# Optimization experiments

Hardware: AMD Instinct MI355X
Metric: run time of the kernel (lower is better)

The kernel has to match this reference:

```python
import jax, jax.numpy as jnp
import numpy as np

DIM = 1024
NUM_EXPERTS = 4
NUM_HEADS = 16
MLP_RATIO = 4
B, N = 8, 1024
EPS = 1e-5


def layernorm(x, w, b):
    mu = jnp.mean(x, axis=-1, keepdims=True)
    var = jnp.mean(jnp.square(x - mu), axis=-1, keepdims=True)
    return (x - mu) * jax.lax.rsqrt(var + EPS) * w + b


def setup_inputs() -> dict:
    key = jax.random.key(0)
    ks = jax.random.split(key, 6)
    x = jax.random.normal(ks[0], (B, N, DIM), dtype=jnp.float32)
    expert_mask = jax.random.randint(ks[1], (B, N), 0, NUM_EXPERTS)
    expert_probs = jax.random.uniform(ks[2], (B, N), dtype=jnp.float32)
    expand_dim = 3 * DIM + MLP_RATIO * DIM
    expand_weight = jax.random.normal(ks[3], (expand_dim, DIM), dtype=jnp.float32) * 0.02
    mlp_bias = jnp.zeros((MLP_RATIO * DIM,), dtype=jnp.float32)
    contract_weight = jax.random.normal(ks[4], (2 * DIM, MLP_RATIO * DIM + DIM), dtype=jnp.float32) * 0.02
    contract_bias = jnp.zeros((2 * DIM,), dtype=jnp.float32)
    norm1_w = jnp.ones((DIM,), dtype=jnp.float32)
    norm1_b = jnp.zeros((DIM,), dtype=jnp.float32)
    norm2_w = jnp.ones((2 * DIM,), dtype=jnp.float32)
    norm2_b = jnp.zeros((2 * DIM,), dtype=jnp.float32)
    return {"x": x, "expert_probs": expert_probs, "expand_weight": expand_weight,
            "mlp_bias": mlp_bias, "contract_weight": contract_weight,
            "contract_bias": contract_bias, "norm1_w": norm1_w, "norm1_b": norm1_b,
            "norm2_w": norm2_w, "norm2_b": norm2_b, "expert_mask": expert_mask}


def reference(x, expert_probs, expand_weight, mlp_bias, contract_weight,
              contract_bias, norm1_w, norm1_b, norm2_w, norm2_b, expert_mask):
    dim = DIM
    # nested sub-dim per token: expert m uses first dim >> (E-1-m) features
    shift = NUM_EXPERTS - 1 - expert_mask                       # (B, N)
    d_in = dim // jnp.left_shift(1, shift)                      # (B, N)
    in_mask = (jnp.arange(dim)[None, None, :] < d_in[..., None]).astype(x.dtype)

    # fused expand bias: [mlp_bias, qkv_bias(=zeros since qkv_bias=False)]
    input_bias = jnp.concatenate([mlp_bias, jnp.zeros((3 * dim,), x.dtype)], axis=-1)

    xn = layernorm(x, norm1_w, norm1_b) * in_mask               # nested_linear_expand input masking
    y = jnp.einsum('bnd,ed->bne', xn, expand_weight) + input_bias  # (B, N, 7*dim)

    qkv, mlp_hidden = y[..., :3 * dim], y[..., 3 * dim:]
    q = qkv[..., :dim]
    kv = layernorm(qkv[..., dim:], norm2_w, norm2_b)            # (B, N, 2*dim)
    k, v = kv[..., :dim], kv[..., dim:]

    # multi-head attention
    dh = dim // NUM_HEADS
    scale = dh ** -0.5
    b, n = x.shape[0], x.shape[1]
    def heads(t):
        return t.reshape(b, n, NUM_HEADS, dh).transpose(0, 2, 1, 3)
    qh, kh, vh = heads(q), heads(k), heads(v)
    attn = jax.nn.softmax(jnp.einsum('bhqd,bhkd->bhqk', qh, kh) * scale, axis=-1)
    attn_output = jnp.einsum('bhqk,bhkd->bhqd', attn, vh).transpose(0, 2, 1, 3).reshape(b, n, dim)

    # nested_linear_contract: full matmul, then mask outputs beyond (2*dim)>>shift
    concat_in = jnp.concatenate([jax.nn.gelu(mlp_hidden, approximate=False), attn_output], axis=-1)
    cy = jnp.einsum('bnc,oc->bno', concat_in, contract_weight) + contract_bias  # (B, N, 2*dim)
    d_out = (2 * dim) // jnp.left_shift(1, shift)
    out_mask = (jnp.arange(2 * dim)[None, None, :] < d_out[..., None]).astype(x.dtype)
    cy = cy * out_mask + jnp.concatenate([x, x], axis=-1)       # residual.repeat(1,1,2)

    mlp_output, attn_out = cy[..., :dim], cy[..., dim:]
    return attn_out + expert_probs[..., None] * mlp_output
```

## Files before the change

kernel.cpp:

```cpp
#include <hip/hip_runtime.h>
#include <cmath>

#define NT    8192
#define DIM_  1024
#define EXP_  7168
#define CD_   5120
#define OD_   2048
#define MPAD  8704
#define NRT   68

typedef __attribute__((ext_vector_type(8))) short short8;
typedef __attribute__((ext_vector_type(4))) float f32x4;
typedef __attribute__((ext_vector_type(4))) unsigned short ushort4_t;

__device__ __forceinline__ unsigned short f2bf(float f) {
  union { float f; unsigned u; } v; v.f = f;
  return (unsigned short)((v.u + 0x7FFFu + ((v.u >> 16) & 1u)) >> 16);
}
__device__ __forceinline__ float bf2f(unsigned short u) {
  union { unsigned u; float f; } v; v.u = ((unsigned)u) << 16;
  return v.f;
}

#define MFMA16(a, b, c) __builtin_amdgcn_mfma_f32_16x16x32_bf16(a, b, c, 0, 0, 0)

__global__ __launch_bounds__(256) void count_experts(const int* __restrict__ em,
                                                     int* __restrict__ blockCnt) {
  __shared__ int h[4];
  int tid = threadIdx.x;
  if (tid < 4) h[tid] = 0;
  __syncthreads();
  atomicAdd(&h[em[blockIdx.x * 256 + tid]], 1);
  __syncthreads();
  if (tid < 4) blockCnt[blockIdx.x * 4 + tid] = h[tid];
}

__global__ void scan_make(const int* __restrict__ blockCnt, int* __restrict__ desc) {
  if (threadIdx.x != 0) return;
  int cnt[4] = {0, 0, 0, 0};
  for (int b = 0; b < 32; b++)
    for (int e = 0; e < 4; e++) cnt[e] += blockCnt[b * 4 + e];
  int base[4]; int acc = 0;
  for (int e = 0; e < 4; e++) { base[e] = acc; acc += ((cnt[e] + 127) >> 7) << 7; }
  for (int e = 0; e < 4; e++) { desc[e] = base[e]; desc[4 + e] = cnt[e]; }
  for (int r = 0; r < NRT; r++) {
    int te = -1;
    for (int e = 0; e < 4; e++) {
      int lo = base[e] >> 7;
      int hi = (base[e] + (((cnt[e] + 127) >> 7) << 7)) >> 7;
      if (r >= lo && r < hi) te = e;
    }
    desc[8 + r] = te;
  }
  int run[4];
  for (int e = 0; e < 4; e++) run[e] = base[e];
  for (int b = 0; b < 32; b++)
    for (int e = 0; e < 4; e++) { desc[76 + b * 4 + e] = run[e]; run[e] += blockCnt[b * 4 + e]; }
}

__global__ __launch_bounds__(256) void fill_perm(int* __restrict__ perm) {
  int i = blockIdx.x * 256 + threadIdx.x;
  if (i < MPAD) perm[i] = -1;
}

__global__ __launch_bounds__(256) void scatter_perm(const int* __restrict__ em,
    const int* __restrict__ desc, int* __restrict__ perm, int* __restrict__ pos) {
  __shared__ int wsum[4][4];
  int tid = threadIdx.x;
  int wv = tid >> 6, ln = tid & 63;
  int t = blockIdx.x * 256 + tid;
  int e = em[t];
  int wrank = 0;
#pragma unroll
  for (int k = 0; k < 4; k++) {
    unsigned long long m = __ballot(e == k);
    if (ln == 0) wsum[wv][k] = __popcll(m);
    if (e == k) wrank = __popcll(m & ((1ull << ln) - 1ull));
  }
  __syncthreads();
  int off = desc[76 + blockIdx.x * 4 + e];
  for (int w = 0; w < wv; w++) off += wsum[w][e];
  int p = off + wrank;
  perm[p] = t;
  pos[t] = p;
}

__global__ __launch_bounds__(256) void cvt_bf16(const float* __restrict__ in,
                                                unsigned short* __restrict__ out, int n) {
  int i = (blockIdx.x * 256 + threadIdx.x) * 4;
  if (i >= n) return;
  float4 v = *(const float4*)(in + i);
  ushort4_t o;
  o[0] = f2bf(v.x); o[1] = f2bf(v.y); o[2] = f2bf(v.z); o[3] = f2bf(v.w);
  *(ushort4_t*)(out + i) = o;
}

__global__ __launch_bounds__(256) void ln1_kernel(const float* __restrict__ x,
    const float* __restrict__ w, const float* __restrict__ b,
    const int* __restrict__ emask, const int* __restrict__ pos,
    unsigned short* __restrict__ xn) {
  int wave = threadIdx.x >> 6, lane = threadIdx.x & 63;
  int t = blockIdx.x * 4 + wave;
  const float* xt = x + (size_t)t * DIM_;
  float4 v[4];
  float s = 0.f, s2 = 0.f;
#pragma unroll
  for (int i = 0; i < 4; i++) {
    v[i] = *(const float4*)(xt + i * 256 + lane * 4);
    s  += v[i].x + v[i].y + v[i].z + v[i].w;
    s2 += v[i].x * v[i].x + v[i].y * v[i].y + v[i].z * v[i].z + v[i].w * v[i].w;
  }
#pragma unroll
  for (int o = 1; o < 64; o <<= 1) { s += __shfl_xor(s, o); s2 += __shfl_xor(s2, o); }
  float mu = s * (1.f / 1024.f);
  float rs = rsqrtf(s2 * (1.f / 1024.f) - mu * mu + 1e-5f);
  int din = 1024 >> (3 - emask[t]);
  unsigned short* ot = xn + (size_t)pos[t] * DIM_;
#pragma unroll
  for (int i = 0; i < 4; i++) {
    int c0 = i * 256 + lane * 4;
    float fv[4] = { v[i].x, v[i].y, v[i].z, v[i].w };
    ushort4_t o;
#pragma unroll
    for (int j = 0; j < 4; j++) {
      int c = c0 + j;
      float val = (c < din) ? (fv[j] - mu) * rs * w[c] + b[c] : 0.f;
      o[j] = f2bf(val);
    }
    *(ushort4_t*)(ot + c0) = o;
  }
}

__global__ __launch_bounds__(256, 3) void gemm_grp1(
    const unsigned short* __restrict__ A, const unsigned short* __restrict__ W,
    const float* __restrict__ bias, const int* __restrict__ tdesc,
    const int* __restrict__ perm, unsigned short* __restrict__ out0,
    unsigned short* __restrict__ out1, unsigned short* __restrict__ out2) {
  __shared__ unsigned short lds[16384];
  unsigned short* As = lds;
  unsigned short* Bs = lds + 8192;
  const int r = blockIdx.y;
  const int e = tdesc[8 + r];
  if (e < 0) return;
  const int ntiles = 4 << e;
  constexpr int KK = 1024;

  const int tid = threadIdx.x;
  const int lane = tid & 63;
  const int wave = tid >> 6;
  const int wm = wave >> 1, wn = wave & 1;
  const int lg = lane >> 4, lr = lane & 15;

  constexpr int CPX = 56 >> 3;
  const int bx = (int)blockIdx.x;
  const int bn = (bx & 7) * CPX + (bx >> 3);
  const int n0 = bn * 128;
  const int m0 = r * 128;

  const int s0g = tid >> 3,        s1g = (256 + tid) >> 3;
  const int lc0 = (tid & 7) ^ (s0g & 7), lc1 = (tid & 7) ^ (s1g & 7);
  const int row0 = 2 * s0g + (lc0 >> 2), kc0 = lc0 & 3;
  const int row1 = 2 * s1g + (lc1 >> 2), kc1 = lc1 & 3;
  const unsigned short* aS0 = A + (size_t)(m0 + row0) * KK + kc0 * 8;
  const unsigned short* aS1 = A + (size_t)(m0 + row1) * KK + kc1 * 8;
  const unsigned short* bS0 = W + (size_t)(n0 + row0) * KK + kc0 * 8;
  const unsigned short* bS1 = W + (size_t)(n0 + row1) * KK + kc1 * 8;

#define GLD(SRC, DST)                                                                \
  __builtin_amdgcn_global_load_lds(                                                  \
      (const __attribute__((address_space(1))) void*)(SRC),                          \
      (__attribute__((address_space(3))) void*)(DST), 16, 0, 0)
#define STAGE(T, SLOT) {                                                             \
    GLD(aS0 + (size_t)(T) * 32, As + (SLOT) * 4096 + tid * 8);                       \
    GLD(aS1 + (size_t)(T) * 32, As + (SLOT) * 4096 + 2048 + tid * 8);                \
    GLD(bS0 + (size_t)(T) * 32, Bs + (SLOT) * 4096 + tid * 8);                       \
    GLD(bS1 + (size_t)(T) * 32, Bs + (SLOT) * 4096 + 2048 + tid * 8);                \
  }

  const int fb = (lr >> 1) * 128 + ((((lr & 1) << 2) + lg) ^ ((lr >> 1) & 7)) * 16;
  const char* apb = (const char*)As + wm * 4096 + fb;
  const char* bpb = (const char*)Bs + wn * 4096 + fb;

  short8 afr[4], bfr[4];
#define LDFRAG(C)                                                                    \
  _Pragma("unroll") for (int mi = 0; mi < 4; mi++)                                   \
    afr[mi] = *(const short8*)(apb + (C) * 8192 + mi * 1024);                        \
  _Pragma("unroll") for (int ni = 0; ni < 4; ni++)                                   \
    bfr[ni] = *(const short8*)(bpb + (C) * 8192 + ni * 1024);

  f32x4 acc[4][4];
  f32x4 zf = { 0.f, 0.f, 0.f, 0.f };
#pragma unroll
  for (int i = 0; i < 4; i++)
#pragma unroll
    for (int j = 0; j < 4; j++) acc[i][j] = zf;

  STAGE(0, 0)
  STAGE(1, 1)
  asm volatile("s_waitcnt vmcnt(4)" ::: "memory");
  __builtin_amdgcn_s_barrier();

#pragma unroll 1
  for (int t = 0; t < ntiles; ++t) {
    const int c = t & 1;
    LDFRAG(c)
    asm volatile("s_waitcnt lgkmcnt(0)" ::: "memory");
    __builtin_amdgcn_sched_barrier(0);
    __builtin_amdgcn_s_barrier();
    const int t2 = (t + 2 < ntiles) ? t + 2 : t;
    STAGE(t2, c)
    __builtin_amdgcn_s_setprio(1);
#pragma unroll
    for (int mi = 0; mi < 4; mi++)
#pragma unroll
      for (int ni = 0; ni < 4; ni++)
        acc[mi][ni] = MFMA16(afr[mi], bfr[ni], acc[mi][ni]);
    __builtin_amdgcn_s_setprio(0);
    asm volatile("s_waitcnt vmcnt(4)" ::: "memory");
    __builtin_amdgcn_s_barrier();
  }
  asm volatile("s_waitcnt vmcnt(0)" ::: "memory");

#pragma unroll
  for (int mi = 0; mi < 4; mi++) {
#pragma unroll
    for (int ni = 0; ni < 4; ni++) {
#pragma unroll
      for (int rr = 0; rr < 4; rr++) {
        int grow = m0 + wm * 64 + mi * 16 + lg * 4 + rr;
        int gcol = n0 + wn * 64 + ni * 16 + lr;
        float v = acc[mi][ni][rr];
        int tk = perm[grow];
        if (tk < 0) continue;
        float bv = bias[gcol & 4095];
        v += (gcol < 4096) ? bv : 0.f;
        if (gcol < 1024) {
          int bb = tk >> 10, n = tk & 1023, h = gcol >> 6, d = gcol & 63;
          out0[(((size_t)(bb * 16 + h) * 1024 + n) << 6) + d] = f2bf(v * 0.125f);
        } else if (gcol < 3072) {
          out1[(size_t)tk * OD_ + (gcol - 1024)] = f2bf(v);
        } else {
          float g = 0.5f * v * (1.f + erff(v * 0.70710678f));
          out2[(size_t)tk * CD_ + (gcol - 3072)] = f2bf(g);
        }
      }
    }
  }
#undef GLD
#undef STAGE
#undef LDFRAG
}

__global__ __launch_bounds__(512, 2) void gemm2_8p(
    const unsigned short* __restrict__ A, const unsigned short* __restrict__ W,
    const float* __restrict__ bias, unsigned short* __restrict__ out0) {
  extern __shared__ unsigned short lds[];
  unsigned short* As = lds;
  unsigned short* Bs = lds + 32768;
  constexpr int KK = 5120;
  constexpr int NTILES = KK / 64;
  const int tid = threadIdx.x;
  const int lane = tid & 63;
  const int wave = tid >> 6;
  const int wm = wave >> 2;
  const int wn = wave & 3;
  const int lg = lane >> 4, lr = lane & 15;

  int cpx = (int)gridDim.x >> 3;
  int lid = ((int)blockIdx.x & 7) * cpx + ((int)blockIdx.x >> 3);
  int bm = lid >> 3, bn = lid & 7;
  int m0 = bm * 256, n0 = bn * 256;

  const int srow = tid >> 3;
  const int schunk = (tid & 7) ^ (srow & 7);
  const unsigned short* aSrc = A + (size_t)(m0 + srow) * KK + schunk * 8;
  const unsigned short* bSrc = W + (size_t)(n0 + srow) * KK + schunk * 8;

  const int xor0 = (lg ^ (lr & 7)) * 8;
  const int xor1 = ((4 + lg) ^ (lr & 7)) * 8;
  const unsigned short* ap0 = As + (wm * 64 + lr) * 64 + xor0;
  const unsigned short* ap1 = As + (wm * 64 + lr) * 64 + xor1;
  const unsigned short* bp0 = Bs + (wn * 32 + lr) * 64 + xor0;
  const unsigned short* bp1 = Bs + (wn * 32 + lr) * 64 + xor1;

#define STAGE_A(TT, SLOT, SEG)                                                       \
  __builtin_amdgcn_global_load_lds(                                                  \
    (const __attribute__((address_space(1))) void*)(aSrc +                           \
      (size_t)(SEG) * 64 * KK + (size_t)(TT) * 64),                                  \
    (__attribute__((address_space(3))) void*)(As + (SLOT) * 16384 +                  \
      (SEG) * 4096 + tid * 8), 16, 0, 0)
#define STAGE_B(TT, SLOT, SEG)                                                       \
  __builtin_amdgcn_global_load_lds(                                                  \
    (const __attribute__((address_space(1))) void*)(bSrc +                           \
      (size_t)(SEG) * 64 * KK + (size_t)(TT) * 64),                                  \
    (__attribute__((address_space(3))) void*)(Bs + (SLOT) * 16384 +                  \
      (SEG) * 4096 + tid * 8), 16, 0, 0)

  short8 afr[4][2], bfr[2][2][2];
#define LDFRAG_A(C, QM)                                                              \
  _Pragma("unroll") for (int mi = 0; mi < 4; mi++) {                                 \
    afr[mi][0] = *(const short8*)(ap0 + (C) * 16384 + (QM) * 8192 + mi * 1024);      \
    afr[mi][1] = *(const short8*)(ap1 + (C) * 16384 + (QM) * 8192 + mi * 1024);      \
  }
#define LDFRAG_B(C, QN)                                                              \
  _Pragma("unroll") for (int ni = 0; ni < 2; ni++) {                                 \
    bfr[QN][ni][0] = *(const short8*)(bp0 + (C) * 16384 + (QN) * 8192 + ni * 1024);  \
    bfr[QN][ni][1] = *(const short8*)(bp1 + (C) * 16384 + (QN) * 8192 + ni * 1024);  \
  }
#define DOMFMA(QM, QN)                                                               \
  __builtin_amdgcn_s_setprio(1);                                                     \
  _Pragma("unroll") for (int mi = 0; mi < 4; mi++)                                   \
  _Pragma("unroll") for (int ni = 0; ni < 2; ni++) {                                 \
    acc[(QM) * 4 + mi][(QN) * 2 + ni] =                                              \
        MFMA16(afr[mi][0], bfr[QN][ni][0], acc[(QM) * 4 + mi][(QN) * 2 + ni]);       \
    acc[(QM) * 4 + mi][(QN) * 2 + ni] =                                              \
        MFMA16(afr[mi][1], bfr[QN][ni][1], acc[(QM) * 4 + mi][(QN) * 2 + ni]);       \
  }                                                                                  \
  __builtin_amdgcn_s_setprio(0);

#define SCHED0 __builtin_amdgcn_sched_barrier(0)

#define TILE_BODY(T, C) {                                                            \
    const int tn1 = ((T) + 1 < NTILES) ? (T) + 1 : NTILES - 1;                       \
    const int tn2 = ((T) + 2 < NTILES) ? (T) + 2 : NTILES - 1;                       \
    LDFRAG_A(C, 0); LDFRAG_B(C, 0);                                                  \
    STAGE_B(tn1, (C) ^ 1, 2); STAGE_B(tn1, (C) ^ 1, 3);                              \
    SCHED0;                                                                          \
    __builtin_amdgcn_s_barrier();                                                    \
    asm volatile("s_waitcnt lgkmcnt(0)");                                            \
    SCHED0;                                                                          \
    DOMFMA(0, 0);                                                                    \
    asm volatile("s_waitcnt vmcnt(6)" ::: "memory");                                 \
    __builtin_amdgcn_s_barrier();                                                    \
    LDFRAG_B(C, 1);                                                                  \
    STAGE_A(tn1, (C) ^ 1, 2); STAGE_A(tn1, (C) ^ 1, 3);                              \
    SCHED0;                                                                          \
    __builtin_amdgcn_s_barrier();                                                    \
    asm volatile("s_waitcnt lgkmcnt(0)");                                            \
    SCHED0;                                                                          \
    DOMFMA(0, 1);                                                                    \
    __builtin_amdgcn_s_barrier();                                                    \
    LDFRAG_A(C, 1);                                                                  \
    STAGE_A(tn2, (C), 0); STAGE_A(tn2, (C), 1);                                      \
    SCHED0;                                                                          \
    __builtin_amdgcn_s_barrier();                                                    \
    asm volatile("s_waitcnt lgkmcnt(0)");                                            \
    SCHED0;                                                                          \
    DOMFMA(1, 0);                                                                    \
    __builtin_amdgcn_s_barrier();                                                    \
    STAGE_B(tn2, (C), 0); STAGE_B(tn2, (C), 1);                                      \
    SCHED0;                                                                          \
    __builtin_amdgcn_s_barrier();                                                    \
    DOMFMA(1, 1);                                                                    \
    asm volatile("s_waitcnt vmcnt(8)" ::: "memory");                                 \
    __builtin_amdgcn_s_barrier();                                                    \
  }

  f32x4 acc[8][4];
  f32x4 zf = { 0.f, 0.f, 0.f, 0.f };
#pragma unroll
  for (int i = 0; i < 8; i++)
#pragma unroll
    for (int j = 0; j < 4; j++) acc[i][j] = zf;

  STAGE_A(0, 0, 0); STAGE_A(0, 0, 1); STAGE_A(0, 0, 2); STAGE_A(0, 0, 3);
  STAGE_B(0, 0, 0); STAGE_B(0, 0, 1); STAGE_B(0, 0, 2); STAGE_B(0, 0, 3);
  STAGE_A(1, 1, 0); STAGE_A(1, 1, 1);
  STAGE_B(1, 1, 0); STAGE_B(1, 1, 1);
  asm volatile("s_waitcnt vmcnt(4)" ::: "memory");
  __builtin_amdgcn_s_barrier();

#pragma unroll 1
  for (int tp = 0; tp < NTILES / 2; ++tp) {
    TILE_BODY(2 * tp, 0)
    TILE_BODY(2 * tp + 1, 1)
  }
  asm volatile("s_waitcnt vmcnt(0)" ::: "memory");

#pragma unroll
  for (int mi8 = 0; mi8 < 8; mi8++) {
#pragma unroll
    for (int nj = 0; nj < 4; nj++) {
#pragma unroll
      for (int r = 0; r < 4; r++) {
        int grow = m0 + wm * 64 + (mi8 >> 2) * 128 + (mi8 & 3) * 16 + lg * 4 + r;
        int gcol = n0 + wn * 32 + (nj >> 1) * 128 + (nj & 1) * 16 + lr;
        float v = acc[mi8][nj][r] + bias[gcol];
        out0[(size_t)grow * OD_ + gcol] = f2bf(v);
      }
    }
  }
#undef STAGE_A
#undef STAGE_B
#undef LDFRAG_A
#undef LDFRAG_B
#undef DOMFMA
#undef SCHED0
#undef TILE_BODY
}

__global__ __launch_bounds__(256) void ln2_kernel(const unsigned short* __restrict__ kv,
    const float* __restrict__ w, const float* __restrict__ b,
    unsigned short* __restrict__ kb, unsigned short* __restrict__ vrm) {
  int wave = threadIdx.x >> 6, lane = threadIdx.x & 63;
  int t = blockIdx.x * 4 + wave;
  const unsigned short* p = kv + (size_t)t * OD_;
  float vals[4][8];
  float s = 0.f, s2 = 0.f;
#pragma unroll
  for (int i = 0; i < 4; i++) {
    short8 v = *(const short8*)(p + i * 512 + lane * 8);
#pragma unroll
    for (int j = 0; j < 8; j++) {
      float f = bf2f((unsigned short)v[j]);
      vals[i][j] = f; s += f; s2 += f * f;
    }
  }
#pragma unroll
  for (int o = 1; o < 64; o <<= 1) { s += __shfl_xor(s, o); s2 += __shfl_xor(s2, o); }
  float mu = s * (1.f / 2048.f);
  float rs = rsqrtf(s2 * (1.f / 2048.f) - mu * mu + 1e-5f);
  int bidx = t >> 10, n = t & 1023;
#pragma unroll
  for (int i = 0; i < 4; i++) {
    int c0 = i * 512 + lane * 8;
    short8 o8;
#pragma unroll
    for (int j = 0; j < 8; j++) {
      int c = c0 + j;
      o8[j] = (short)f2bf((vals[i][j] - mu) * rs * w[c] + b[c]);
    }
    if (c0 < 1024) {
      int h = c0 >> 6, d = c0 & 63;
      *(short8*)(kb + (((size_t)(bidx * 16 + h) * 1024 + n) << 6) + d) = o8;
    } else {
      *(short8*)(vrm + (size_t)t * 1024 + (c0 - 1024)) = o8;
    }
  }
}

__global__ __launch_bounds__(256) void transpose_v(const unsigned short* __restrict__ vrm,
                                                   unsigned short* __restrict__ vt) {
  int bh = blockIdx.x >> 4;
  int nblk = (blockIdx.x & 15) * 64;
  int b = bh >> 4, h = bh & 15;
  __shared__ unsigned short tile[64][65];
  int tid = threadIdx.x;
  int i = tid >> 2;
  int d0 = (tid & 3) * 16;
  const unsigned short* src = vrm + ((size_t)(b * 1024 + nblk + i)) * 1024 + h * 64 + d0;
  short8 v0 = *(const short8*)(src);
  short8 v1 = *(const short8*)(src + 8);
#pragma unroll
  for (int j = 0; j < 8; j++) {
    tile[d0 + j][i] = (unsigned short)v0[j];
    tile[d0 + 8 + j][i] = (unsigned short)v1[j];
  }
  __syncthreads();
  int d = tid >> 2;
  int i0 = (tid & 3) * 16;
  unsigned short* dst = vt + ((size_t)bh * 64 + d) * 1024 + nblk + i0;
  short8 o0, o1;
#pragma unroll
  for (int j = 0; j < 8; j++) { o0[j] = (short)tile[d][i0 + j]; o1[j] = (short)tile[d][i0 + 8 + j]; }
  *(short8*)dst = o0;
  *(short8*)(dst + 8) = o1;
}

__global__ __launch_bounds__(64) void attn_kernel(const unsigned short* __restrict__ q,
    const unsigned short* __restrict__ k, const unsigned short* __restrict__ vt,
    unsigned short* __restrict__ concat) {
  int bh = blockIdx.x >> 5;
  int q0 = (blockIdx.x & 31) * 32;
  int lane = threadIdx.x;
  int lg = lane >> 4, lr = lane & 15;
  __shared__ unsigned short plds[2][512];
  const unsigned short* qp = q + (size_t)bh * (1024 * 64);
  const unsigned short* kp = k + (size_t)bh * (1024 * 64);
  const unsigned short* vp = vt + (size_t)bh * (64 * 1024);
  short8 qf[2][2];
#pragma unroll
  for (int rb = 0; rb < 2; rb++)
#pragma unroll
    for (int c = 0; c < 2; c++)
      qf[rb][c] = *(const short8*)(qp + (q0 + rb * 16 + lr) * 64 + c * 32 + lg * 8);
  f32x4 zf = { 0.f, 0.f, 0.f, 0.f };
  f32x4 o[2][4];
  float m[2][4], l[2][4];
#pragma unroll
  for (int rb = 0; rb < 2; rb++) {
#pragma unroll
    for (int r = 0; r < 4; r++) { m[rb][r] = -1e30f; l[rb][r] = 0.f; }
#pragma unroll
    for (int nb = 0; nb < 4; nb++) o[rb][nb] = zf;
  }
  for (int kt = 0; kt < 1024; kt += 32) {
    f32x4 s[2][2];
    s[0][0] = zf; s[0][1] = zf; s[1][0] = zf; s[1][1] = zf;
#pragma unroll
    for (int h2 = 0; h2 < 2; h2++) {
      short8 kf0 = *(const short8*)(kp + (kt + h2 * 16 + lr) * 64 + lg * 8);
      short8 kf1 = *(const short8*)(kp + (kt + h2 * 16 + lr) * 64 + 32 + lg * 8);
      s[0][h2] = MFMA16(qf[0][0], kf0, s[0][h2]);
      s[0][h2] = MFMA16(qf[0][1], kf1, s[0][h2]);
      s[1][h2] = MFMA16(qf[1][0], kf0, s[1][h2]);
      s[1][h2] = MFMA16(qf[1][1], kf1, s[1][h2]);
    }
    __syncthreads();
#pragma unroll
    for (int rb = 0; rb < 2; rb++) {
      float mx[4], rsum[4];
#pragma unroll
      for (int r = 0; r < 4; r++) mx[r] = fmaxf(s[rb][0][r], s[rb][1][r]);
#pragma unroll
      for (int ofs = 1; ofs < 16; ofs <<= 1)
#pragma unroll
        for (int r = 0; r < 4; r++) mx[r] = fmaxf(mx[r], __shfl_xor(mx[r], ofs));
#pragma unroll
      for (int r = 0; r < 4; r++) {
        float mn = fmaxf(m[rb][r], mx[r]);
        float al = __expf(m[rb][r] - mn);
        float p0 = __expf(s[rb][0][r] - mn);
        float p1 = __expf(s[rb][1][r] - mn);
        m[rb][r] = mn;
        plds[rb][(lg * 4 + r) * 32 + lr] = f2bf(p0);
        plds[rb][(lg * 4 + r) * 32 + 16 + lr] = f2bf(p1);
        rsum[r] = p0 + p1;
        l[rb][r] *= al;
#pragma unroll
        for (int nb = 0; nb < 4; nb++) o[rb][nb][r] *= al;
      }
#pragma unroll
      for (int ofs = 1; ofs < 16; ofs <<= 1)
#pragma unroll
        for (int r = 0; r < 4; r++) rsum[r] += __shfl_xor(rsum[r], ofs);
#pragma unroll
      for (int r = 0; r < 4; r++) l[rb][r] += rsum[r];
    }
    __syncthreads();
    short8 pf0 = *(const short8*)(&plds[0][lr * 32 + lg * 8]);
    short8 pf1 = *(const short8*)(&plds[1][lr * 32 + lg * 8]);
#pragma unroll
    for (int nb = 0; nb < 4; nb++) {
      short8 vf = *(const short8*)(vp + (nb * 16 + lr) * 1024 + kt + lg * 8);
      o[0][nb] = MFMA16(pf0, vf, o[0][nb]);
      o[1][nb] = MFMA16(pf1, vf, o[1][nb]);
    }
  }
  int b = bh >> 4, h = bh & 15;
#pragma unroll
  for (int rb = 0; rb < 2; rb++)
#pragma unroll
    for (int r = 0; r < 4; r++) {
      int n = q0 + rb * 16 + lg * 4 + r;
      size_t t = (size_t)b * 1024 + n;
      float inv = 1.f / l[rb][r];
#pragma unroll
      for (int nb = 0; nb < 4; nb++)
        concat[t * CD_ + 4096 + h * 64 + nb * 16 + lr] = f2bf(o[rb][nb][r] * inv);
    }
}

__global__ __launch_bounds__(256) void final_epi(const unsigned short* __restrict__ cy,
    const float* __restrict__ x, const float* __restrict__ probs,
    const int* __restrict__ emask, float* __restrict__ out) {
  int t = blockIdx.x;
  int c = threadIdx.x * 4;
  int dout = 2048 >> (3 - emask[t]);
  float p = probs[t];
  const unsigned short* cyt = cy + (size_t)t * OD_;
  ushort4_t mv = *(const ushort4_t*)(cyt + c);
  ushort4_t av = *(const ushort4_t*)(cyt + 1024 + c);
  float4 xv = *(const float4*)(x + (size_t)t * 1024 + c);
  float xa[4] = { xv.x, xv.y, xv.z, xv.w };
  float4 o;
  float oa[4];
#pragma unroll
  for (int j = 0; j < 4; j++) {
    float mlp = ((c + j) < dout ? bf2f(mv[j]) : 0.f) + xa[j];
    float att = ((1024 + c + j) < dout ? bf2f(av[j]) : 0.f) + xa[j];
    oa[j] = att + p * mlp;
  }
  o.x = oa[0]; o.y = oa[1]; o.z = oa[2]; o.w = oa[3];
  *(float4*)(out + (size_t)t * 1024 + c) = o;
}

extern "C" void kernel_launch(void* const* d_in, const int* in_sizes, int n_in,
                              void* d_out, int out_size, void* d_ws, size_t ws_size,
                              hipStream_t stream) {
  const float* x        = (const float*)d_in[0];
  const float* probs    = (const float*)d_in[1];
  const float* we       = (const float*)d_in[2];
  const float* mlp_bias = (const float*)d_in[3];
  const float* wc       = (const float*)d_in[4];
  const float* cbias    = (const float*)d_in[5];
  const float* n1w      = (const float*)d_in[6];
  const float* n1b      = (const float*)d_in[7];
  const float* n2w      = (const float*)d_in[8];
  const float* n2b      = (const float*)d_in[9];
  const int*   emask    = (const int*)d_in[10];
  float* out = (float*)d_out;

  char* ws = (char*)d_ws;
  size_t off = 0;
  auto alloc = [&](size_t bytes) {
    char* p = ws + off;
    off += (bytes + 255) & ~(size_t)255;
    return p;
  };
  unsigned short* we_bf = (unsigned short*)alloc((size_t)EXP_ * DIM_ * 2);
  unsigned short* wc_bf = (unsigned short*)alloc((size_t)OD_ * CD_ * 2);
  unsigned short* xn    = (unsigned short*)alloc((size_t)MPAD * DIM_ * 2);
  unsigned short* qb    = (unsigned short*)alloc((size_t)NT * DIM_ * 2);
  unsigned short* kv    = (unsigned short*)alloc((size_t)NT * OD_ * 2);
  unsigned short* kb    = (unsigned short*)alloc((size_t)NT * DIM_ * 2);
  unsigned short* vt    = (unsigned short*)alloc((size_t)NT * DIM_ * 2);
  unsigned short* cc    = (unsigned short*)alloc((size_t)NT * CD_ * 2);
  int* blockCnt         = (int*)alloc(32 * 4 * 4);
  int* desc             = (int*)alloc(256 * 4);
  int* perm             = (int*)alloc(MPAD * 4);
  int* pos              = (int*)alloc(NT * 4);
  unsigned short* vrm = xn;
  unsigned short* cy  = kv;
  if (off > ws_size) return;

  hipFuncSetAttribute((const void*)gemm2_8p,
                      hipFuncAttributeMaxDynamicSharedMemorySize, 131072);

  count_experts<<<32, 256, 0, stream>>>(emask, blockCnt);
  scan_make<<<1, 64, 0, stream>>>(blockCnt, desc);
  fill_perm<<<34, 256, 0, stream>>>(perm);
  scatter_perm<<<32, 256, 0, stream>>>(emask, desc, perm, pos);

  cvt_bf16<<<7168, 256, 0, stream>>>(we, we_bf, EXP_ * DIM_);
  cvt_bf16<<<10240, 256, 0, stream>>>(wc, wc_bf, OD_ * CD_);
  ln1_kernel<<<2048, 256, 0, stream>>>(x, n1w, n1b, emask, pos, xn);
  gemm_grp1<<<dim3(56, NRT), 256, 0, stream>>>(xn, we_bf, mlp_bias, desc,
                                               perm, qb, kv, cc);
  ln2_kernel<<<2048, 256, 0, stream>>>(kv, n2w, n2b, kb, vrm);
  transpose_v<<<2048, 256, 0, stream>>>(vrm, vt);
  attn_kernel<<<4096, 64, 0, stream>>>(qb, kb, vt, cc);
  gemm2_8p<<<256, 512, 131072, stream>>>(cc, wc_bf, cbias, cy);
  final_epi<<<8192, 256, 0, stream>>>(cy, x, probs, emask, out);
}
```

Measured before the change: 506.1 us.

## Pack four attention waves per block, drop barriers, lazy rescale, swizzle P LDS

The attention kernel now runs four independent 64-lane waves per 256-thread block, each handling 32 queries of the same head with its own private P staging area. The block-wide barriers are replaced by a per-wave lgkmcnt wait. The online softmax skips the running-max rescale unless the new max exceeds the old one by more than 8, and the P tile in LDS is written with an XOR-style swizzle to reduce bank conflicts. Dropping the barrier relies on the whole exchange staying inside one wavefront. The lazy rescale lets exponentials reach up to e^8, which could stress bf16 precision slightly.

```diff
diff --git a/kernel.cpp b/kernel.cpp
--- a/kernel.cpp
+++ b/kernel.cpp
@@ -467,14 +467,16 @@
   *(short8*)(dst + 8) = o1;
 }
 
-__global__ __launch_bounds__(64) void attn_kernel(const unsigned short* __restrict__ q,
+__global__ __launch_bounds__(256) void attn_kernel(const unsigned short* __restrict__ q,
     const unsigned short* __restrict__ k, const unsigned short* __restrict__ vt,
     unsigned short* __restrict__ concat) {
-  int bh = blockIdx.x >> 5;
-  int q0 = (blockIdx.x & 31) * 32;
-  int lane = threadIdx.x;
+  int bh = blockIdx.x >> 3;
+  int wv = threadIdx.x >> 6;
+  int q0 = (blockIdx.x & 7) * 128 + wv * 32;
+  int lane = threadIdx.x & 63;
   int lg = lane >> 4, lr = lane & 15;
-  __shared__ unsigned short plds[2][512];
+  __shared__ unsigned short plds[4][2][512];
+  unsigned short* pw = &plds[wv][0][0];
   const unsigned short* qp = q + (size_t)bh * (1024 * 64);
   const unsigned short* kp = k + (size_t)bh * (1024 * 64);
   const unsigned short* vp = vt + (size_t)bh * (64 * 1024);
@@ -494,6 +496,7 @@
 #pragma unroll
     for (int nb = 0; nb < 4; nb++) o[rb][nb] = zf;
   }
+  const int prd = lr * 32 + (((lg + lr) & 3) << 3);
   for (int kt = 0; kt < 1024; kt += 32) {
     f32x4 s[2][2];
     s[0][0] = zf; s[0][1] = zf; s[1][0] = zf; s[1][1] = zf;
@@ -506,7 +509,6 @@
       s[1][h2] = MFMA16(qf[1][0], kf0, s[1][h2]);
       s[1][h2] = MFMA16(qf[1][1], kf1, s[1][h2]);
     }
-    __syncthreads();
 #pragma unroll
     for (int rb = 0; rb < 2; rb++) {
       float mx[4], rsum[4];
@@ -516,19 +518,28 @@
       for (int ofs = 1; ofs < 16; ofs <<= 1)
 #pragma unroll
         for (int r = 0; r < 4; r++) mx[r] = fmaxf(mx[r], __shfl_xor(mx[r], ofs));
+      bool need = false;
+#pragma unroll
+      for (int r = 0; r < 4; r++) need |= (mx[r] > m[rb][r] + 8.f);
+      if (need) {
+#pragma unroll
+        for (int r = 0; r < 4; r++) {
+          float mn = fmaxf(m[rb][r], mx[r]);
+          float al = __expf(m[rb][r] - mn);
+          m[rb][r] = mn;
+          l[rb][r] *= al;
+#pragma unroll
+          for (int nb = 0; nb < 4; nb++) o[rb][nb][r] *= al;
+        }
+      }
 #pragma unroll
       for (int r = 0; r < 4; r++) {
-        float mn = fmaxf(m[rb][r], mx[r]);
-        float al = __expf(m[rb][r] - mn);
-        float p0 = __expf(s[rb][0][r] - mn);
-        float p1 = __expf(s[rb][1][r] - mn);
-        m[rb][r] = mn;
-        plds[rb][(lg * 4 + r) * 32 + lr] = f2bf(p0);
-        plds[rb][(lg * 4 + r) * 32 + 16 + lr] = f2bf(p1);
+        float p0 = __expf(s[rb][0][r] - m[rb][r]);
+        float p1 = __expf(s[rb][1][r] - m[rb][r]);
+        int q_ = lg * 4 + r;
+        pw[rb * 512 + q_ * 32 + ((((lr >> 3) + q_) & 3) << 3) + (lr & 7)] = f2bf(p0);
+        pw[rb * 512 + q_ * 32 + (((2 + (lr >> 3) + q_) & 3) << 3) + (lr & 7)] = f2bf(p1);
         rsum[r] = p0 + p1;
-        l[rb][r] *= al;
-#pragma unroll
-        for (int nb = 0; nb < 4; nb++) o[rb][nb][r] *= al;
       }
 #pragma unroll
       for (int ofs = 1; ofs < 16; ofs <<= 1)
@@ -537,9 +548,9 @@
 #pragma unroll
       for (int r = 0; r < 4; r++) l[rb][r] += rsum[r];
     }
-    __syncthreads();
-    short8 pf0 = *(const short8*)(&plds[0][lr * 32 + lg * 8]);
-    short8 pf1 = *(const short8*)(&plds[1][lr * 32 + lg * 8]);
+    asm volatile("s_waitcnt lgkmcnt(0)" ::: "memory");
+    short8 pf0 = *(const short8*)(pw + prd);
+    short8 pf1 = *(const short8*)(pw + 512 + prd);
 #pragma unroll
     for (int nb = 0; nb < 4; nb++) {
       short8 vf = *(const short8*)(vp + (nb * 16 + lr) * 1024 + kt + lg * 8);
@@ -639,7 +650,7 @@
                                                perm, qb, kv, cc);
   ln2_kernel<<<2048, 256, 0, stream>>>(kv, n2w, n2b, kb, vrm);
   transpose_v<<<2048, 256, 0, stream>>>(vrm, vt);
-  attn_kernel<<<4096, 64, 0, stream>>>(qb, kb, vt, cc);
+  attn_kernel<<<1024, 256, 0, stream>>>(qb, kb, vt, cc);
   gemm2_8p<<<256, 512, 131072, stream>>>(cc, wc_bf, cbias, cy);
   final_epi<<<8192, 256, 0, stream>>>(cy, x, probs, emask, out);
 }
```

Result: no change. 506.1 us (-0.0%).
